# Kernel tuning notes

Hardware: AMD Instinct MI355X
Metric: run time of the kernel (lower is better)

Reference implementation:

```python
import jax, jax.numpy as jnp
import numpy as np

FP8_MAX = 448.0  # float8_e4m3fn max
EPS = 1e-6


def _rms_norm(x, w):
    # x: [T, H], w: [H]
    var = jnp.mean(x * x, axis=-1, keepdims=True)
    return x * jax.lax.rsqrt(var + EPS) * w


def _fused_add_rms_norm(x, resid, w):
    r = x + resid
    return _rms_norm(r, w), r


def _fp8_linear(y, W):
    # dynamic per-token activation quant + per-tensor weight quant, fp8 e4m3
    s = jnp.maximum(jnp.max(jnp.abs(y), axis=-1, keepdims=True) / FP8_MAX, 1e-12)  # [T,1]
    qx = jnp.clip(y / s, -FP8_MAX, FP8_MAX).astype(jnp.float8_e4m3fn).astype(jnp.float32)
    ws = jnp.maximum(jnp.max(jnp.abs(W)) / FP8_MAX, 1e-12)  # scalar
    qw = jnp.clip(W / ws, -FP8_MAX, FP8_MAX).astype(jnp.float8_e4m3fn).astype(jnp.float32)
    # out = dequant(qx) @ dequant(qw).T = (qx @ qw.T) * s * ws ; W is [out, in]
    return (qx @ qw.T) * (s * ws)


def setup_inputs() -> dict:
    key = jax.random.key(0)
    ks = jax.random.split(key, 8)
    H, T = 4096, 4096
    x = jax.random.normal(ks[0], (T, H), dtype=jnp.float32)
    nw0 = 1.0 + 0.02 * jax.random.normal(ks[1], (H,), dtype=jnp.float32)
    nw1 = 1.0 + 0.02 * jax.random.normal(ks[2], (H,), dtype=jnp.float32)
    nw2 = 1.0 + 0.02 * jax.random.normal(ks[3], (H,), dtype=jnp.float32)
    nw3 = 1.0 + 0.02 * jax.random.normal(ks[4], (H,), dtype=jnp.float32)
    W0 = 0.02 * jax.random.normal(ks[5], (H, H), dtype=jnp.float32)
    W1 = 0.02 * jax.random.normal(ks[6], (H, H), dtype=jnp.float32)
    W2 = 0.02 * jax.random.normal(ks[7], (H, H), dtype=jnp.float32)
    return {"x": x, "nw0": nw0, "nw1": nw1, "nw2": nw2, "nw3": nw3,
            "W0": W0, "W1": W1, "W2": W2}


def reference(x, nw0, nw1, nw2, nw3, W0, W1, W2):
    x = jax.nn.relu(x)
    resid = x
    y = _rms_norm(x, nw0)
    x2 = _fp8_linear(y, W0)
    y2, resid = _fused_add_rms_norm(x2, resid, nw1)
    x3 = _fp8_linear(y2, W1)
    y3, resid = _fused_add_rms_norm(x3, resid, nw2)
    x4 = _fp8_linear(y3, W2)
    y4, resid = _fused_add_rms_norm(x4, resid, nw3)
    return y4
```

## Files before the change

kernel.cpp:

```cpp
#include <hip/hip_runtime.h>
#include <cstdint>
#include <cstddef>

#define AS1 __attribute__((address_space(1)))
#define AS3 __attribute__((address_space(3)))

typedef __attribute__((ext_vector_type(4))) float f32x4;
typedef __attribute__((ext_vector_type(16))) float f32x16;
typedef __attribute__((ext_vector_type(4))) int i32x4;
typedef __attribute__((ext_vector_type(8))) int i32x8;

constexpr int HD = 4096;
constexpr float FP8MAX = 448.0f;

__device__ inline uint32_t pack4_fp8(float a, float b, float c, float d) {
    int v = 0;
    v = __builtin_amdgcn_cvt_pk_fp8_f32(a, b, v, false);
    v = __builtin_amdgcn_cvt_pk_fp8_f32(c, d, v, true);
    return (uint32_t)v;
}

__device__ inline float clipmul(float y, float rcs) {
    float t = y * rcs;
    t = fminf(t, FP8MAX);
    t = fmaxf(t, -FP8MAX);
    return t;
}

__device__ inline uint32_t quant4(float4 v, float rcs) {
    return pack4_fp8(clipmul(v.x, rcs), clipmul(v.y, rcs),
                     clipmul(v.z, rcs), clipmul(v.w, rcs));
}

__global__ __launch_bounds__(256) void w_absmax(const float* __restrict__ W0,
                                                const float* __restrict__ W1,
                                                const float* __restrict__ W2,
                                                uint32_t* __restrict__ wmax) {
    __shared__ float red[4];
    const float* W = (blockIdx.z == 0) ? W0 : (blockIdx.z == 1 ? W1 : W2);
    const float4* W4 = (const float4*)W;
    const int n4 = HD * HD / 4;
    float m = 0.f;
    for (int i = blockIdx.x * blockDim.x + threadIdx.x; i < n4; i += gridDim.x * blockDim.x) {
        float4 v = W4[i];
        m = fmaxf(m, fmaxf(fmaxf(fabsf(v.x), fabsf(v.y)), fmaxf(fabsf(v.z), fabsf(v.w))));
    }
#pragma unroll
    for (int i = 32; i > 0; i >>= 1) m = fmaxf(m, __shfl_xor(m, i, 64));
    if ((threadIdx.x & 63) == 0) red[threadIdx.x >> 6] = m;
    __syncthreads();
    if (threadIdx.x == 0) {
        m = fmaxf(fmaxf(red[0], red[1]), fmaxf(red[2], red[3]));
        atomicMax((unsigned int*)(wmax + blockIdx.z), __float_as_uint(m));
    }
}

__global__ __launch_bounds__(256) void w_quant(const float* __restrict__ W,
                                               const uint32_t* __restrict__ wmaxbits,
                                               uint32_t* __restrict__ qw) {
    const float rsw = 1.0f / fmaxf(__uint_as_float(*wmaxbits) / FP8MAX, 1e-12f);
    const int i = blockIdx.x * blockDim.x + threadIdx.x;
    qw[i] = quant4(((const float4*)W)[i], rsw);
}

__global__ __launch_bounds__(256) void fused_rms(const float* __restrict__ xin,
                                                 const float* __restrict__ addin,
                                                 float* __restrict__ resid_out,
                                                 const float* __restrict__ nw,
                                                 uint32_t* __restrict__ qx,
                                                 float* __restrict__ srow,
                                                 float* __restrict__ yout,
                                                 const int mode,
                                                 const float* __restrict__ Wq,
                                                 const uint32_t* __restrict__ wqmaxbits,
                                                 uint32_t* __restrict__ qwout) {
    const int tid = threadIdx.x;
    if (blockIdx.x >= 4096) {
        const float rsw = 1.0f / fmaxf(__uint_as_float(*wqmaxbits) / FP8MAX, 1e-12f);
        const float4* W4 = (const float4*)Wq;
        int i = (blockIdx.x - 4096) * 256 + tid;
#pragma unroll
        for (int it = 0; it < 4; it++, i += 4096 * 256)
            qwout[i] = quant4(W4[i], rsw);
        return;
    }

    __shared__ float reds[4];
    __shared__ float redm[4];
    const int row = blockIdx.x;
    const size_t base = (size_t)row * HD;
    const float4* xr = (const float4*)(xin + base);
    const float4* nw4 = (const float4*)nw;

    float4 v[4], w[4];
    float ss = 0.f, pm = 0.f;
    if (mode == 0) {
#pragma unroll
        for (int j = 0; j < 4; j++) {
            float4 t = xr[tid + j * 256];
            w[j] = nw4[tid + j * 256];
            t.x = fmaxf(t.x, 0.f); t.y = fmaxf(t.y, 0.f);
            t.z = fmaxf(t.z, 0.f); t.w = fmaxf(t.w, 0.f);
            v[j] = t;
            ss += t.x * t.x + t.y * t.y + t.z * t.z + t.w * t.w;
            pm = fmaxf(pm, fmaxf(fmaxf(fabsf(t.x * w[j].x), fabsf(t.y * w[j].y)),
                                 fmaxf(fabsf(t.z * w[j].z), fabsf(t.w * w[j].w))));
        }
    } else {
        const float4* ar = (const float4*)(addin + base);
#pragma unroll
        for (int j = 0; j < 4; j++) {
            float4 t = xr[tid + j * 256];
            float4 a = ar[tid + j * 256];
            w[j] = nw4[tid + j * 256];
            t.x += a.x; t.y += a.y; t.z += a.z; t.w += a.w;
            v[j] = t;
            ss += t.x * t.x + t.y * t.y + t.z * t.z + t.w * t.w;
            pm = fmaxf(pm, fmaxf(fmaxf(fabsf(t.x * w[j].x), fabsf(t.y * w[j].y)),
                                 fmaxf(fabsf(t.z * w[j].z), fabsf(t.w * w[j].w))));
        }
    }
    if (resid_out) {
        float4* ro = (float4*)(resid_out + base);
#pragma unroll
        for (int j = 0; j < 4; j++) ro[tid + j * 256] = v[j];
    }

#pragma unroll
    for (int i = 32; i > 0; i >>= 1) {
        ss += __shfl_xor(ss, i, 64);
        pm = fmaxf(pm, __shfl_xor(pm, i, 64));
    }
    if ((tid & 63) == 0) { reds[tid >> 6] = ss; redm[tid >> 6] = pm; }
    __syncthreads();
    ss = (reds[0] + reds[1]) + (reds[2] + reds[3]);
    pm = fmaxf(fmaxf(redm[0], redm[1]), fmaxf(redm[2], redm[3]));

    const float rs = 1.0f / sqrtf(ss / (float)HD + 1e-6f);

    if (mode == 2) {
        float4* yo = (float4*)(yout + base);
#pragma unroll
        for (int j = 0; j < 4; j++) {
            float4 t;
            t.x = (v[j].x * rs) * w[j].x; t.y = (v[j].y * rs) * w[j].y;
            t.z = (v[j].z * rs) * w[j].z; t.w = (v[j].w * rs) * w[j].w;
            yo[tid + j * 256] = t;
        }
        return;
    }

    const float amax = pm * rs;
    const float s = fmaxf(amax / FP8MAX, 1e-12f);
    const float rcs = 1.0f / s;
    if (tid == 0) srow[row] = s;
    uint32_t* qr = qx + base / 4;
#pragma unroll
    for (int j = 0; j < 4; j++) {
        float4 t;
        t.x = (v[j].x * rs) * w[j].x; t.y = (v[j].y * rs) * w[j].y;
        t.z = (v[j].z * rs) * w[j].z; t.w = (v[j].w * rs) * w[j].w;
        qr[tid + j * 256] = quant4(t, rcs);
    }
}

typedef union { i32x8 v8; i32x4 v4[2]; } frag8;

__global__ __launch_bounds__(512, 2) void gemm_fp8mx(const uint8_t* __restrict__ qx,
                                                     const uint8_t* __restrict__ qw,
                                                     const float* __restrict__ srow,
                                                     const uint32_t* __restrict__ wmaxbits,
                                                     float* __restrict__ out) {
    __shared__ i32x4 AsL[2][2][1024];
    __shared__ i32x4 BsL[2][2][1024];

    const int tid = threadIdx.x;
    const int wave = tid >> 6, lane = tid & 63;
    const int lr = lane & 31, lh = lane >> 5;
    const int m0 = blockIdx.y * 256, n0 = blockIdx.x * 256;
    const int wm = (wave >> 2) * 128, wn = (wave & 3) * 64;

    const int str = tid >> 2;
    const int skg = (tid & 3) ^ ((str >> 1) & 3);
    const size_t srcA = (size_t)(m0 + str) * HD + (size_t)(skg * 16);
    const size_t srcB = (size_t)(n0 + str) * HD + (size_t)(skg * 16);

    f32x16 acc[4][2];
#pragma unroll
    for (int i = 0; i < 4; i++)
#pragma unroll
        for (int j = 0; j < 2; j++)
#pragma unroll
            for (int e = 0; e < 16; e++) acc[i][j][e] = 0.f;

    frag8 af0, af1, af2, af3, bf0, bf1;

#define STAGE_U(gp, soff, larr, koff) do {                                              \
    __builtin_amdgcn_global_load_lds((const AS1 void*)((gp) + (soff) + (size_t)(koff)), \
                                     (AS3 void*)((larr) + tid), 16, 0, 0);              \
    __builtin_amdgcn_global_load_lds((const AS1 void*)((gp) + (soff) + (size_t)(koff) + 128u * HD), \
                                     (AS3 void*)((larr) + 512 + tid), 16, 0, 0);        \
} while (0)

#define READ_F(dst, rbase, larr) do {                 \
    const int r_ = (rbase);                           \
    const i32x4* p_ = (larr) + r_ * 4;                \
    const int sw_ = (r_ >> 1) & 3;                    \
    dst.v4[0] = p_[(lh * 2) ^ sw_];                   \
    dst.v4[1] = p_[(lh * 2 + 1) ^ sw_];               \
} while (0)

#define MFMA1(a_, b_, i_, j_)                                                            \
    acc[i_][j_] = __builtin_amdgcn_mfma_scale_f32_32x32x64_f8f6f4(                       \
        (a_).v8, (b_).v8, acc[i_][j_], 0, 0, 0, 0x7F7F7F7Fu, 0, 0x7F7F7F7Fu)

#define MFMA4(a0_, a1_, r0_, r1_) do {               \
    __builtin_amdgcn_s_setprio(1);                   \
    MFMA1(a0_, bf0, r0_, 0);                         \
    MFMA1(a0_, bf1, r0_, 1);                         \
    MFMA1(a1_, bf0, r1_, 0);                         \
    MFMA1(a1_, bf1, r1_, 1);                         \
    __builtin_amdgcn_s_setprio(0);                   \
} while (0)

#define KTILE(bR, bS, knext) do {                                   \
                       \
    READ_F(af0, wm + lr,      &AsL[bR][0][0]);                      \
    READ_F(af1, wm + 32 + lr, &AsL[bR][0][0]);                      \
    READ_F(bf0, wn + lr,      &BsL[bR][0][0]);                      \
    READ_F(bf1, wn + 32 + lr, &BsL[bR][0][0]);                      \
    STAGE_U(qx, srcA, &AsL[bS][0][0], (knext));                     \
    __builtin_amdgcn_s_barrier();                                   \
    MFMA4(af0, af1, 0, 1);                                          \
    __builtin_amdgcn_s_barrier();                                   \
                     \
    READ_F(af2, wm + 64 + lr, &AsL[bR][0][0]);                      \
    READ_F(af3, wm + 96 + lr, &AsL[bR][0][0]);                      \
    STAGE_U(qw, srcB, &BsL[bS][0][0], (knext));                     \
    __builtin_amdgcn_s_barrier();                                   \
    MFMA4(af2, af3, 2, 3);                                          \
    asm volatile("s_waitcnt vmcnt(4)" ::: "memory");                \
    __builtin_amdgcn_s_barrier();                                   \
                       \
    READ_F(af0, wm + lr,      &AsL[bR][1][0]);                      \
    READ_F(af1, wm + 32 + lr, &AsL[bR][1][0]);                      \
    READ_F(bf0, wn + lr,      &BsL[bR][1][0]);                      \
    READ_F(bf1, wn + 32 + lr, &BsL[bR][1][0]);                      \
    STAGE_U(qx, srcA, &AsL[bS][1][0], (knext) + 64);                \
    __builtin_amdgcn_s_barrier();                                   \
    MFMA4(af0, af1, 0, 1);                                          \
    __builtin_amdgcn_s_barrier();                                   \
                     \
    READ_F(af2, wm + 64 + lr, &AsL[bR][1][0]);                      \
    READ_F(af3, wm + 96 + lr, &AsL[bR][1][0]);                      \
    STAGE_U(qw, srcB, &BsL[bS][1][0], (knext) + 64);                \
    __builtin_amdgcn_s_barrier();                                   \
    MFMA4(af2, af3, 2, 3);                                          \
    asm volatile("s_waitcnt vmcnt(4)" ::: "memory");                \
    __builtin_amdgcn_s_barrier();                                   \
} while (0)

    STAGE_U(qx, srcA, &AsL[0][0][0], 0);
    STAGE_U(qw, srcB, &BsL[0][0][0], 0);
    STAGE_U(qx, srcA, &AsL[0][1][0], 64);
    STAGE_U(qw, srcB, &BsL[0][1][0], 64);
    asm volatile("s_waitcnt vmcnt(4)" ::: "memory");
    __builtin_amdgcn_s_barrier();

#pragma unroll 1
    for (int kt = 0; kt < 32; kt += 2) {
        KTILE(0, 1, (kt + 1) * 128);
        KTILE(1, 0, ((kt + 2) & 31) * 128);
    }

    const float wsc = fmaxf(__uint_as_float(*wmaxbits) / FP8MAX, 1e-12f);
#pragma unroll
    for (int i = 0; i < 4; i++) {
#pragma unroll
        for (int reg = 0; reg < 16; reg++) {
            const int row = (reg & 3) + 8 * (reg >> 2) + 4 * lh;
            const int m = m0 + wm + i * 32 + row;
            const float sv = srow[m] * wsc;
            float* orow = out + (size_t)m * HD + n0 + wn + lr;
#pragma unroll
            for (int j = 0; j < 2; j++)
                orow[j * 32] = acc[i][j][reg] * sv;
        }
    }
#undef KTILE
#undef MFMA4
#undef MFMA1
#undef READ_F
#undef STAGE_U
}

extern "C" void kernel_launch(void* const* d_in, const int* in_sizes, int n_in,
                              void* d_out, int out_size, void* d_ws, size_t ws_size,
                              hipStream_t stream) {
    const float* x   = (const float*)d_in[0];
    const float* nw0 = (const float*)d_in[1];
    const float* nw1 = (const float*)d_in[2];
    const float* nw2 = (const float*)d_in[3];
    const float* nw3 = (const float*)d_in[4];
    const float* W0  = (const float*)d_in[5];
    const float* W1  = (const float*)d_in[6];
    const float* W2  = (const float*)d_in[7];
    float* out = (float*)d_out;

    char* ws = (char*)d_ws;
    const size_t MB = 1024 * 1024;
    float* x2 = out;

    const bool overlap = ws_size >= 118 * MB;

    if (overlap) {
        float*    resid = (float*)(ws);
        uint32_t* qx    = (uint32_t*)(ws + 64 * MB);
        uint32_t* qwA   = (uint32_t*)(ws + 80 * MB);
        uint32_t* qwB   = (uint32_t*)(ws + 96 * MB);
        float*    srow  = (float*)(ws + 112 * MB);
        uint32_t* wmax  = (uint32_t*)(ws + 112 * MB + 16384);

        hipMemsetAsync(wmax, 0, 12, stream);
        hipLaunchKernelGGL(w_absmax, dim3(1024, 1, 3), dim3(256), 0, stream, W0, W1, W2, wmax);

        hipLaunchKernelGGL(fused_rms, dim3(8192), dim3(256), 0, stream,
                           x, (const float*)nullptr, resid, nw0, qx, srow, (float*)nullptr, 0,
                           W0, wmax + 0, qwA);
        hipLaunchKernelGGL(gemm_fp8mx, dim3(16, 16), dim3(512), 0, stream,
                           (const uint8_t*)qx, (const uint8_t*)qwA, srow, wmax + 0, x2);
        hipLaunchKernelGGL(fused_rms, dim3(8192), dim3(256), 0, stream,
                           x2, (const float*)resid, resid, nw1, qx, srow, (float*)nullptr, 1,
                           W1, wmax + 1, qwB);
        hipLaunchKernelGGL(gemm_fp8mx, dim3(16, 16), dim3(512), 0, stream,
                           (const uint8_t*)qx, (const uint8_t*)qwB, srow, wmax + 1, x2);
        hipLaunchKernelGGL(fused_rms, dim3(8192), dim3(256), 0, stream,
                           x2, (const float*)resid, resid, nw2, qx, srow, (float*)nullptr, 1,
                           W2, wmax + 2, qwA);
        hipLaunchKernelGGL(gemm_fp8mx, dim3(16, 16), dim3(512), 0, stream,
                           (const uint8_t*)qx, (const uint8_t*)qwA, srow, wmax + 2, x2);
        hipLaunchKernelGGL(fused_rms, dim3(4096), dim3(256), 0, stream,
                           x2, (const float*)resid, (float*)nullptr, nw3,
                           (uint32_t*)nullptr, (float*)nullptr, out, 2,
                           (const float*)nullptr, (const uint32_t*)nullptr, (uint32_t*)nullptr);
    } else {
        float*    resid = (float*)(ws);
        uint32_t* qx    = (uint32_t*)(ws + 64 * MB);
        uint32_t* qw    = (uint32_t*)(ws + 80 * MB);
        float*    srow  = (float*)(ws + 96 * MB);
        uint32_t* wmax  = (uint32_t*)(ws + 96 * MB + 16384);

        hipMemsetAsync(wmax, 0, 12, stream);
        hipLaunchKernelGGL(w_absmax, dim3(1024, 1, 3), dim3(256), 0, stream, W0, W1, W2, wmax);
        hipLaunchKernelGGL(fused_rms, dim3(4096), dim3(256), 0, stream,
                           x, (const float*)nullptr, resid, nw0, qx, srow, (float*)nullptr, 0,
                           (const float*)nullptr, (const uint32_t*)nullptr, (uint32_t*)nullptr);
        const float* Ws[3]  = {W0, W1, W2};
        const float* nws[3] = {nw1, nw2, nw3};
        for (int l = 0; l < 3; l++) {
            hipLaunchKernelGGL(w_quant, dim3(HD * HD / 4 / 256), dim3(256), 0, stream,
                               Ws[l], wmax + l, qw);
            hipLaunchKernelGGL(gemm_fp8mx, dim3(16, 16), dim3(512), 0, stream,
                               (const uint8_t*)qx, (const uint8_t*)qw, srow, wmax + l, x2);
            if (l < 2) {
                hipLaunchKernelGGL(fused_rms, dim3(4096), dim3(256), 0, stream,
                                   x2, (const float*)resid, resid, nws[l], qx, srow,
                                   (float*)nullptr, 1,
                                   (const float*)nullptr, (const uint32_t*)nullptr, (uint32_t*)nullptr);
            } else {
                hipLaunchKernelGGL(fused_rms, dim3(4096), dim3(256), 0, stream,
                                   x2, (const float*)resid, (float*)nullptr, nws[l],
                                   (uint32_t*)nullptr, (float*)nullptr, out, 2,
                                   (const float*)nullptr, (const uint32_t*)nullptr, (uint32_t*)nullptr);
            }
        }
    }
}
```

Measured before the change: 621.0 us.

## Fold W1/W2 absmax into first RMS launch and restructure GEMM K-loop pipeline

The weight absmax pass now runs only over W0 up front. The W1 and W2 absmax reductions are appended as 1024 extra blocks of the first fused_rms launch, so they overlap with the row normalization instead of running as a separate serial pass. Separately, the GEMM inner loop now issues all four stage loads at the start of each K tile and then runs two uninterrupted 8-MFMA halves. This replaces the earlier interleaving with many barriers and partial vmcnt waits. It cuts barrier count but waits for all loads at the end of each tile, which can expose memory latency.

```diff
diff --git a/kernel.cpp b/kernel.cpp
--- a/kernel.cpp
+++ b/kernel.cpp
@@ -30,6 +30,10 @@
 __device__ inline uint32_t quant4(float4 v, float rcs) {
     return pack4_fp8(clipmul(v.x, rcs), clipmul(v.y, rcs),
                      clipmul(v.z, rcs), clipmul(v.w, rcs));
+}
+
+__device__ inline float max4(float4 v) {
+    return fmaxf(fmaxf(fabsf(v.x), fabsf(v.y)), fmaxf(fabsf(v.z), fabsf(v.w)));
 }
 
 __global__ __launch_bounds__(256) void w_absmax(const float* __restrict__ W0,
@@ -42,8 +46,7 @@
     const int n4 = HD * HD / 4;
     float m = 0.f;
     for (int i = blockIdx.x * blockDim.x + threadIdx.x; i < n4; i += gridDim.x * blockDim.x) {
-        float4 v = W4[i];
-        m = fmaxf(m, fmaxf(fmaxf(fabsf(v.x), fabsf(v.y)), fmaxf(fabsf(v.z), fabsf(v.w))));
+        m = fmaxf(m, max4(W4[i]));
     }
 #pragma unroll
     for (int i = 32; i > 0; i >>= 1) m = fmaxf(m, __shfl_xor(m, i, 64));
@@ -52,6 +55,36 @@
     if (threadIdx.x == 0) {
         m = fmaxf(fmaxf(red[0], red[1]), fmaxf(red[2], red[3]));
         atomicMax((unsigned int*)(wmax + blockIdx.z), __float_as_uint(m));
+    }
+}
+
+__global__ __launch_bounds__(256) void w_absmax1(const float* __restrict__ W,
+                                                 uint32_t* __restrict__ slot) {
+    __shared__ float red[4];
+    const float4* W4 = (const float4*)W;
+    const int stride = 2048 * 256;
+    int i = blockIdx.x * 256 + threadIdx.x;
+    float a0 = 0.f, a1 = 0.f, a2 = 0.f, a3 = 0.f;
+#pragma unroll
+    for (int it = 0; it < 2; it++) {
+        float4 v0 = W4[i];
+        float4 v1 = W4[i + stride];
+        float4 v2 = W4[i + 2 * stride];
+        float4 v3 = W4[i + 3 * stride];
+        a0 = fmaxf(a0, max4(v0));
+        a1 = fmaxf(a1, max4(v1));
+        a2 = fmaxf(a2, max4(v2));
+        a3 = fmaxf(a3, max4(v3));
+        i += 4 * stride;
+    }
+    float m = fmaxf(fmaxf(a0, a1), fmaxf(a2, a3));
+#pragma unroll
+    for (int s = 32; s > 0; s >>= 1) m = fmaxf(m, __shfl_xor(m, s, 64));
+    if ((threadIdx.x & 63) == 0) red[threadIdx.x >> 6] = m;
+    __syncthreads();
+    if (threadIdx.x == 0) {
+        m = fmaxf(fmaxf(red[0], red[1]), fmaxf(red[2], red[3]));
+        atomicMax((unsigned int*)slot, __float_as_uint(m));
     }
 }
 
@@ -73,8 +106,47 @@
                                                  const int mode,
                                                  const float* __restrict__ Wq,
                                                  const uint32_t* __restrict__ wqmaxbits,
-                                                 uint32_t* __restrict__ qwout) {
+                                                 uint32_t* __restrict__ qwout,
+                                                 const float* __restrict__ Wa1,
+                                                 const float* __restrict__ Wa2,
+                                                 uint32_t* __restrict__ wmaxbase) {
     const int tid = threadIdx.x;
+    __shared__ float reds[4];
+    __shared__ float redm[4];
+
+    if (blockIdx.x >= 8192) {
+        const int b = blockIdx.x - 8192;
+        const float* W = (b < 512) ? Wa1 : Wa2;
+        uint32_t* slot = wmaxbase + ((b < 512) ? 1 : 2);
+        const int bb = b & 511;
+        const float4* W4 = (const float4*)W;
+        const int stride = 512 * 256;
+        int i = bb * 256 + tid;
+        float a0 = 0.f, a1 = 0.f, a2 = 0.f, a3 = 0.f;
+#pragma unroll
+        for (int it = 0; it < 8; it++) {
+            float4 v0 = W4[i];
+            float4 v1 = W4[i + stride];
+            float4 v2 = W4[i + 2 * stride];
+            float4 v3 = W4[i + 3 * stride];
+            a0 = fmaxf(a0, max4(v0));
+            a1 = fmaxf(a1, max4(v1));
+            a2 = fmaxf(a2, max4(v2));
+            a3 = fmaxf(a3, max4(v3));
+            i += 4 * stride;
+        }
+        float m = fmaxf(fmaxf(a0, a1), fmaxf(a2, a3));
+#pragma unroll
+        for (int s = 32; s > 0; s >>= 1) m = fmaxf(m, __shfl_xor(m, s, 64));
+        if ((tid & 63) == 0) reds[tid >> 6] = m;
+        __syncthreads();
+        if (tid == 0) {
+            m = fmaxf(fmaxf(reds[0], reds[1]), fmaxf(reds[2], reds[3]));
+            atomicMax((unsigned int*)slot, __float_as_uint(m));
+        }
+        return;
+    }
+
     if (blockIdx.x >= 4096) {
         const float rsw = 1.0f / fmaxf(__uint_as_float(*wqmaxbits) / FP8MAX, 1e-12f);
         const float4* W4 = (const float4*)Wq;
@@ -85,8 +157,6 @@
         return;
     }
 
-    __shared__ float reds[4];
-    __shared__ float redm[4];
     const int row = blockIdx.x;
     const size_t base = (size_t)row * HD;
     const float4* xr = (const float4*)(xin + base);
@@ -214,58 +284,40 @@
     acc[i_][j_] = __builtin_amdgcn_mfma_scale_f32_32x32x64_f8f6f4(                       \
         (a_).v8, (b_).v8, acc[i_][j_], 0, 0, 0, 0x7F7F7F7Fu, 0, 0x7F7F7F7Fu)
 
-#define MFMA4(a0_, a1_, r0_, r1_) do {               \
-    __builtin_amdgcn_s_setprio(1);                   \
-    MFMA1(a0_, bf0, r0_, 0);                         \
-    MFMA1(a0_, bf1, r0_, 1);                         \
-    MFMA1(a1_, bf0, r1_, 0);                         \
-    MFMA1(a1_, bf1, r1_, 1);                         \
-    __builtin_amdgcn_s_setprio(0);                   \
+#define HALF(bR, kh) do {                                           \
+    READ_F(af0, wm + lr,      &AsL[bR][kh][0]);                     \
+    READ_F(af1, wm + 32 + lr, &AsL[bR][kh][0]);                     \
+    READ_F(bf0, wn + lr,      &BsL[bR][kh][0]);                     \
+    READ_F(bf1, wn + 32 + lr, &BsL[bR][kh][0]);                     \
+    READ_F(af2, wm + 64 + lr, &AsL[bR][kh][0]);                     \
+    READ_F(af3, wm + 96 + lr, &AsL[bR][kh][0]);                     \
+    __builtin_amdgcn_s_setprio(1);                                  \
+    MFMA1(af0, bf0, 0, 0); MFMA1(af0, bf1, 0, 1);                   \
+    MFMA1(af1, bf0, 1, 0); MFMA1(af1, bf1, 1, 1);                   \
+    MFMA1(af2, bf0, 2, 0); MFMA1(af2, bf1, 2, 1);                   \
+    MFMA1(af3, bf0, 3, 0); MFMA1(af3, bf1, 3, 1);                   \
+    __builtin_amdgcn_s_setprio(0);                                  \
 } while (0)
 
 #define KTILE(bR, bS, knext) do {                                   \
-                       \
-    READ_F(af0, wm + lr,      &AsL[bR][0][0]);                      \
-    READ_F(af1, wm + 32 + lr, &AsL[bR][0][0]);                      \
-    READ_F(bf0, wn + lr,      &BsL[bR][0][0]);                      \
-    READ_F(bf1, wn + 32 + lr, &BsL[bR][0][0]);                      \
     STAGE_U(qx, srcA, &AsL[bS][0][0], (knext));                     \
+    STAGE_U(qx, srcA, &AsL[bS][1][0], (knext) + 64);                \
+    STAGE_U(qw, srcB, &BsL[bS][0][0], (knext));                     \
+    STAGE_U(qw, srcB, &BsL[bS][1][0], (knext) + 64);                \
+    HALF(bR, 0);                                                    \
+    HALF(bR, 1);                                                    \
+    asm volatile("s_waitcnt vmcnt(0)" ::: "memory");                \
     __builtin_amdgcn_s_barrier();                                   \
-    MFMA4(af0, af1, 0, 1);                                          \
-    __builtin_amdgcn_s_barrier();                                   \
-                     \
-    READ_F(af2, wm + 64 + lr, &AsL[bR][0][0]);                      \
-    READ_F(af3, wm + 96 + lr, &AsL[bR][0][0]);                      \
-    STAGE_U(qw, srcB, &BsL[bS][0][0], (knext));                     \
-    __builtin_amdgcn_s_barrier();                                   \
-    MFMA4(af2, af3, 2, 3);                                          \
-    asm volatile("s_waitcnt vmcnt(4)" ::: "memory");                \
-    __builtin_amdgcn_s_barrier();                                   \
-                       \
-    READ_F(af0, wm + lr,      &AsL[bR][1][0]);                      \
-    READ_F(af1, wm + 32 + lr, &AsL[bR][1][0]);                      \
-    READ_F(bf0, wn + lr,      &BsL[bR][1][0]);                      \
-    READ_F(bf1, wn + 32 + lr, &BsL[bR][1][0]);                      \
-    STAGE_U(qx, srcA, &AsL[bS][1][0], (knext) + 64);                \
-    __builtin_amdgcn_s_barrier();                                   \
-    MFMA4(af0, af1, 0, 1);                                          \
-    __builtin_amdgcn_s_barrier();                                   \
-                     \
-    READ_F(af2, wm + 64 + lr, &AsL[bR][1][0]);                      \
-    READ_F(af3, wm + 96 + lr, &AsL[bR][1][0]);                      \
-    STAGE_U(qw, srcB, &BsL[bS][1][0], (knext) + 64);                \
-    __builtin_amdgcn_s_barrier();                                   \
-    MFMA4(af2, af3, 2, 3);                                          \
-    asm volatile("s_waitcnt vmcnt(4)" ::: "memory");                \
-    __builtin_amdgcn_s_barrier();                                   \
+    __builtin_amdgcn_sched_barrier(0);                              \
 } while (0)
 
     STAGE_U(qx, srcA, &AsL[0][0][0], 0);
+    STAGE_U(qx, srcA, &AsL[0][1][0], 64);
     STAGE_U(qw, srcB, &BsL[0][0][0], 0);
-    STAGE_U(qx, srcA, &AsL[0][1][0], 64);
     STAGE_U(qw, srcB, &BsL[0][1][0], 64);
-    asm volatile("s_waitcnt vmcnt(4)" ::: "memory");
+    asm volatile("s_waitcnt vmcnt(0)" ::: "memory");
     __builtin_amdgcn_s_barrier();
+    __builtin_amdgcn_sched_barrier(0);
 
 #pragma unroll 1
     for (int kt = 0; kt < 32; kt += 2) {
@@ -288,7 +340,7 @@
         }
     }
 #undef KTILE
-#undef MFMA4
+#undef HALF
 #undef MFMA1
 #undef READ_F
 #undef STAGE_U
@@ -322,27 +374,30 @@
         uint32_t* wmax  = (uint32_t*)(ws + 112 * MB + 16384);
 
         hipMemsetAsync(wmax, 0, 12, stream);
-        hipLaunchKernelGGL(w_absmax, dim3(1024, 1, 3), dim3(256), 0, stream, W0, W1, W2, wmax);
-
-        hipLaunchKernelGGL(fused_rms, dim3(8192), dim3(256), 0, stream,
+        hipLaunchKernelGGL(w_absmax1, dim3(2048), dim3(256), 0, stream, W0, wmax + 0);
+
+        hipLaunchKernelGGL(fused_rms, dim3(9216), dim3(256), 0, stream,
                            x, (const float*)nullptr, resid, nw0, qx, srow, (float*)nullptr, 0,
-                           W0, wmax + 0, qwA);
+                           W0, wmax + 0, qwA, W1, W2, wmax);
         hipLaunchKernelGGL(gemm_fp8mx, dim3(16, 16), dim3(512), 0, stream,
                            (const uint8_t*)qx, (const uint8_t*)qwA, srow, wmax + 0, x2);
         hipLaunchKernelGGL(fused_rms, dim3(8192), dim3(256), 0, stream,
                            x2, (const float*)resid, resid, nw1, qx, srow, (float*)nullptr, 1,
-                           W1, wmax + 1, qwB);
+                           W1, wmax + 1, qwB,
+                           (const float*)nullptr, (const float*)nullptr, (uint32_t*)nullptr);
         hipLaunchKernelGGL(gemm_fp8mx, dim3(16, 16), dim3(512), 0, stream,
                            (const uint8_t*)qx, (const uint8_t*)qwB, srow, wmax + 1, x2);
         hipLaunchKernelGGL(fused_rms, dim3(8192), dim3(256), 0, stream,
                            x2, (const float*)resid, resid, nw2, qx, srow, (float*)nullptr, 1,
-                           W2, wmax + 2, qwA);
+                           W2, wmax + 2, qwA,
+                           (const float*)nullptr, (const float*)nullptr, (uint32_t*)nullptr);
         hipLaunchKernelGGL(gemm_fp8mx, dim3(16, 16), dim3(512), 0, stream,
                            (const uint8_t*)qx, (const uint8_t*)qwA, srow, wmax + 2, x2);
         hipLaunchKernelGGL(fused_rms, dim3(4096), dim3(256), 0, stream,
                            x2, (const float*)resid, (float*)nullptr, nw3,
                            (uint32_t*)nullptr, (float*)nullptr, out, 2,
-                           (const float*)nullptr, (const uint32_t*)nullptr, (uint32_t*)nullptr);
+                           (const float*)nullptr, (const uint32_t*)nullptr, (uint32_t*)nullptr,
+                           (const float*)nullptr, (const float*)nullptr, (uint32_t*)nullptr);
     } else {
         float*    resid = (float*)(ws);
         uint32_t* qx    = (uint32_t*)(ws + 64 * MB);
@@ -354,7 +409,8 @@
         hipLaunchKernelGGL(w_absmax, dim3(1024, 1, 3), dim3(256), 0, stream, W0, W1, W2, wmax);
         hipLaunchKernelGGL(fused_rms, dim3(4096), dim3(256), 0, stream,
                            x, (const float*)nullptr, resid, nw0, qx, srow, (float*)nullptr, 0,
-                           (const float*)nullptr, (const uint32_t*)nullptr, (uint32_t*)nullptr);
+                           (const float*)nullptr, (const uint32_t*)nullptr, (uint32_t*)nullptr,
+                           (const float*)nullptr, (const float*)nullptr, (uint32_t*)nullptr);
         const float* Ws[3]  = {W0, W1, W2};
         const float* nws[3] = {nw1, nw2, nw3};
         for (int l = 0; l < 3; l++) {
@@ -366,12 +422,14 @@
                 hipLaunchKernelGGL(fused_rms, dim3(4096), dim3(256), 0, stream,
                                    x2, (const float*)resid, resid, nws[l], qx, srow,
                                    (float*)nullptr, 1,
-                                   (const float*)nullptr, (const uint32_t*)nullptr, (uint32_t*)nullptr);
+                                   (const float*)nullptr, (const uint32_t*)nullptr, (uint32_t*)nullptr,
+                                   (const float*)nullptr, (const float*)nullptr, (uint32_t*)nullptr);
             } else {
                 hipLaunchKernelGGL(fused_rms, dim3(4096), dim3(256), 0, stream,
                                    x2, (const float*)resid, (float*)nullptr, nws[l],
                                    (uint32_t*)nullptr, (float*)nullptr, out, 2,
-                                   (const float*)nullptr, (const uint32_t*)nullptr, (uint32_t*)nullptr);
+                                   (const float*)nullptr, (const uint32_t*)nullptr, (uint32_t*)nullptr,
+                                   (const float*)nullptr, (const float*)nullptr, (uint32_t*)nullptr);
             }
         }
     }
```

Result: no change. 625.7 us (+0.8%).
